# Kernel tuning notes

Measured on AMD Instinct MI355X. Metric: run time of the kernel, lower is better.

The kernel has to match this reference:

```python
import jax, jax.numpy as jnp
import numpy as np

KMAX = 16
NEG_INF = -1e9


def setup_inputs() -> dict:
    key = jax.random.key(0)
    ks = jax.random.split(key, 8)
    B, N, H = 65536, 512, 256
    L = KMAX + 1
    actions = jax.random.randint(ks[0], (B, L), 0, N + 1)  # values in [0, N], N == STOP
    rp = jax.random.uniform(ks[1], (B, 1), dtype=jnp.float32)
    s1 = 1.0 / np.sqrt(N + 3)
    s2 = 1.0 / np.sqrt(H)
    W1 = jax.random.normal(ks[2], (N + 3, H), dtype=jnp.float32) * s1
    b1 = jax.random.normal(ks[3], (H,), dtype=jnp.float32) * 0.01
    W2 = jax.random.normal(ks[4], (H, H), dtype=jnp.float32) * s2
    b2 = jax.random.normal(ks[5], (H,), dtype=jnp.float32) * 0.01
    Wh = jax.random.normal(ks[6], (H, N + 1), dtype=jnp.float32) * s2
    bh = jax.random.normal(ks[7], (N + 1,), dtype=jnp.float32) * 0.01
    return {"actions": actions, "rp": rp, "W1": W1, "b1": b1, "W2": W2, "b2": b2, "Wh": Wh, "bh": bh}


def reference(actions, rp, W1, b1, W2, b2, Wh, bh):
    B, L = actions.shape
    N = Wh.shape[1] - 1
    f32 = rp.dtype

    def step_fn(carry, a):
        sel_mask, k_sel, step, logpf = carry  # [B,N], [B,1], [B,1], [B]
        x = jnp.concatenate([sel_mask, k_sel, step, rp], axis=-1)  # [B, N+3]
        h = jax.nn.relu(x @ W1 + b1)
        h = jax.nn.relu(h @ W2 + b2)
        logits = h @ Wh + bh  # [B, N+1]
        k = k_sel[:, 0]
        full = (k >= KMAX).astype(f32)[:, None]
        mask_assets = (1.0 - sel_mask) * (1.0 - full)  # cannot re-add or exceed Kmax
        mask_stop = (k > 0).astype(f32)[:, None]       # cannot STOP on empty set
        mask = jnp.concatenate([mask_assets, mask_stop], axis=-1)
        logits = jnp.where(mask <= 0.0, NEG_INF, logits)
        logp = jax.nn.log_softmax(logits, axis=-1)
        alive = a >= 0
        a_safe = jnp.clip(a, 0, N)
        chosen = jnp.take_along_axis(logp, a_safe[:, None], axis=-1)[:, 0]
        logpf = logpf + jnp.where(alive, chosen, 0.0)
        stop = (a == N) & alive
        add = (alive & (~stop)).astype(f32)[:, None]
        # one_hot of N/-1 is all-zero, so only valid adds update sel_mask
        upd = jax.nn.one_hot(a_safe, N, dtype=f32) * add
        sel_mask = jnp.maximum(sel_mask, upd)
        k_sel = jnp.sum(sel_mask, axis=-1, keepdims=True)
        step = step + 1.0
        return (sel_mask, k_sel, step, logpf), None

    init = (jnp.zeros((B, N), f32), jnp.zeros((B, 1), f32), jnp.zeros((B, 1), f32), jnp.zeros((B,), f32))
    (_, _, _, logpf), _ = jax.lax.scan(step_fn, init, actions.T)  # scan over L steps
    return logpf
```

## Files before the change

kernel.cpp:

```cpp
#include <hip/hip_runtime.h>


#define NEG_INF (-1000000000.0f)
#define LOG2E 1.4426950408889634f
#define LN2   0.6931471805599453f

#define A_NEW  0x400

#define HST 1040
#define HKT 2080

typedef short bf16x8 __attribute__((ext_vector_type(8)));
typedef float f32x16 __attribute__((ext_vector_type(16)));

__device__ __forceinline__ unsigned short f2bf(float x){
  unsigned int u = __float_as_uint(x);
  u = (u + 0x7FFFu + ((u >> 16) & 1u)) >> 16;
  return (unsigned short)u;
}
__device__ __forceinline__ float bf2f(unsigned short h){
  return __uint_as_float(((unsigned int)h) << 16);
}
__device__ __forceinline__ unsigned int cvt_pk_bf16(float lo, float hi){
  unsigned int r;
  asm("v_cvt_pk_bf16_f32 %0, %1, %2" : "=v"(r) : "v"(lo), "v"(hi));
  return r;
}
__device__ __forceinline__ float4 ld4bf(const unsigned short* p){
  ushort4 u = *(const ushort4*)p;
  return make_float4(bf2f(u.x), bf2f(u.y), bf2f(u.z), bf2f(u.w));
}

__global__ void prep_kernel(const float* __restrict__ W2, const float* __restrict__ Wh,
                            unsigned short* __restrict__ w2f, unsigned short* __restrict__ whf,
                            float* __restrict__ whstop){
  int id = blockIdx.x * 256 + threadIdx.x;
  if (id < 8192){
    int lane = id & 63; int tile = id >> 6;
    int ntg = tile >> 4, kt = tile & 15;
    int col = ntg * 32 + (lane & 31);
    int k0  = kt * 16 + (lane >> 5) * 8;
    unsigned int u[4];
#pragma unroll
    for (int p = 0; p < 4; ++p){
      unsigned short lo = f2bf(W2[(k0 + 2*p    ) * 256 + col]);
      unsigned short hi = f2bf(W2[(k0 + 2*p + 1) * 256 + col]);
      u[p] = (unsigned int)lo | ((unsigned int)hi << 16);
    }
    *(uint4*)(w2f + (size_t)id * 8) = make_uint4(u[0], u[1], u[2], u[3]);
  } else if (id < 24576){
    int id2 = id - 8192;
    int lane = id2 & 63; int tile = id2 >> 6;
    int pt = tile >> 4, kt = tile & 15;
    int col = pt * 32 + (lane & 31);
    int k0  = kt * 16 + (lane >> 5) * 8;
    unsigned int u[4];
#pragma unroll
    for (int p = 0; p < 4; ++p){
      unsigned short lo = f2bf(Wh[(k0 + 2*p    ) * 513 + col] * LOG2E);
      unsigned short hi = f2bf(Wh[(k0 + 2*p + 1) * 513 + col] * LOG2E);
      u[p] = (unsigned int)lo | ((unsigned int)hi << 16);
    }
    *(uint4*)(whf + (size_t)id2 * 8) = make_uint4(u[0], u[1], u[2], u[3]);
  } else if (id < 24832){
    int k = id - 24576;
    whstop[k] = Wh[k * 513 + 512];
  }
}

__launch_bounds__(256, 4)
__global__ void gfn_kernel(const int* __restrict__ actions, const float* __restrict__ rp,
                           const float* __restrict__ W1, const float* __restrict__ b1,
                           const float* __restrict__ b2, const float* __restrict__ bh,
                           const unsigned short* __restrict__ w2f,
                           const unsigned short* __restrict__ whf,
                           const float* __restrict__ whstop,
                           float* __restrict__ out)
{
  __shared__ alignas(16) char h[32 * HST];
  __shared__ alignas(16) unsigned short c16[1024];
  __shared__ alignas(16) float bhl2[512];
  __shared__ alignas(16) float b2s[256];
  __shared__ alignas(16) unsigned short whst_h[256];
  __shared__ alignas(16) unsigned short amask[18][32];
  __shared__ alignas(16) float predsum[64];
  __shared__ alignas(16) float stopp[64];
  __shared__ alignas(16) unsigned short chosen16[64];

  const int tid  = threadIdx.x;
  const int wave = tid >> 6;
  const int lane = tid & 63;
  const int ln5  = lane & 31;
  const int lg2  = lane >> 5;
  const int base = blockIdx.x * 32;

  for (int i = tid; i < 1024; i += 256){
    int rrow = i >> 8, f = i & 255;
    float v = (rrow < 3) ? W1[(512 + rrow) * 256 + f] : b1[f];
    c16[i] = f2bf(v);
  }
  b2s[tid] = b2[tid];
  whst_h[tid] = f2bf(whstop[tid]);
  for (int i = tid; i < 512; i += 256){
    int pt = i >> 5, l2 = (i >> 4) & 1, r = i & 15;
    int col = pt * 32 + (r & 3) + 8 * (r >> 2) + 4 * l2;
    bhl2[i] = bh[col] * LOG2E;
  }
  const float stopbias = bh[512];
  if (tid < 64){ stopp[tid] = 0.f; predsum[tid] = 0.f; }
  int* acts = (int*)h;
  for (int i = tid; i < 544; i += 256) acts[i] = actions[base * 17 + i];
  float logpf = 0.f;
  uint4 selw_r = make_uint4(0u, 0u, 0u, 0u);
  __syncthreads();

  if (tid < 32){
    int s = tid, k = 0;
    for (int t = 0; t < 17; ++t){
      int a = acts[s * 17 + t];
      bool alive = (a >= 0);
      bool isnew = alive && (a < 512);
      if (isnew){
        for (int u = 0; u < t; ++u) if (acts[s * 17 + u] == a){ isnew = false; break; }
      }
      int av = alive ? a : 1023;
      amask[t][s] = (unsigned short)(av | (isnew ? A_NEW : 0) | (k << 11));
      if (isnew) ++k;
    }
    amask[17][s] = (unsigned short)(1023 | (k << 11));
  }
  unsigned int Spk[16];
#pragma unroll
  for (int j = 0; j < 16; ++j) Spk[j] = 0u;
  __syncthreads();

  const int aw_base = (lane >> 1) * HST + (lane & 1) * 8 + wave * 128;
  const int br_base = lg2 * HST;
  const int bw_base = wave * 8 * HST + lg2 * 8;
  const int cr_base = lg2 * HST + ln5 * 16;
  const int rpu = __builtin_amdgcn_readfirstlane(base + wave * 8);
  const unsigned lane8 = (unsigned)lane * 8u;
  const unsigned short* w2p0 = w2f + (unsigned)(wave * 2    ) * 8192u + lane8;
  const unsigned short* w2p1 = w2f + (unsigned)(wave * 2 + 1) * 8192u + lane8;

#pragma unroll 1
  for (int c = 0; c < 9; ++c){
    const int t = c * 2;

    {
      const float4 ck4 = ld4bf(&c16[lane * 4]);
      const float4 ct4 = ld4bf(&c16[256 + lane * 4]);
      const float4 cr4 = ld4bf(&c16[512 + lane * 4]);
      const float4 cb4 = ld4bf(&c16[768 + lane * 4]);
      float tf = (float)t;
      float c00 = cb4.x + tf * ct4.x, c01 = cb4.y + tf * ct4.y;
      float c02 = cb4.z + tf * ct4.z, c03 = cb4.w + tf * ct4.w;
#pragma unroll
      for (int s8 = 0; s8 < 8; ++s8){
        int s = wave * 8 + s8;
        float rv = rp[rpu + s8];
        int m0 = amask[t][s];
        int m1 = amask[t + 1][s];
        unsigned int pk0 = Spk[s8 * 2], pk1 = Spk[s8 * 2 + 1];
        float S0 = __uint_as_float(pk0 << 16);
        float S1 = __uint_as_float(pk0 & 0xFFFF0000u);
        float S2 = __uint_as_float(pk1 << 16);
        float S3 = __uint_as_float(pk1 & 0xFFFF0000u);
        float kf = (float)(m0 >> 11);
        float v0 = S0 + kf * ck4.x + rv * cr4.x + c00;
        float v1 = S1 + kf * ck4.y + rv * cr4.y + c01;
        float v2 = S2 + kf * ck4.z + rv * cr4.z + c02;
        float v3 = S3 + kf * ck4.w + rv * cr4.w + c03;
        *(uint2*)(h + aw_base + s8 * 16) =
            make_uint2(cvt_pk_bf16(fmaxf(v0,0.f), fmaxf(v1,0.f)),
                       cvt_pk_bf16(fmaxf(v2,0.f), fmaxf(v3,0.f)));
        float d0 = ct4.x, d1 = ct4.y, d2 = ct4.z, d3 = ct4.w;
        if (m0 & A_NEW){
          int a = m0 & 1023;
          float4 w = *(const float4*)(W1 + (size_t)a * 256 + lane * 4);
          S0 += w.x; S1 += w.y; S2 += w.z; S3 += w.w;
          d0 += w.x + ck4.x; d1 += w.y + ck4.y; d2 += w.z + ck4.z; d3 += w.w + ck4.w;
        }
        v0 += d0; v1 += d1; v2 += d2; v3 += d3;
        *(uint2*)(h + aw_base + 512 + s8 * 16) =
            make_uint2(cvt_pk_bf16(fmaxf(v0,0.f), fmaxf(v1,0.f)),
                       cvt_pk_bf16(fmaxf(v2,0.f), fmaxf(v3,0.f)));
        if (m1 & A_NEW){
          int a = m1 & 1023;
          float4 w = *(const float4*)(W1 + (size_t)a * 256 + lane * 4);
          S0 += w.x; S1 += w.y; S2 += w.z; S3 += w.w;
        }
        if ((m0 | m1) & A_NEW){
          Spk[s8 * 2]     = cvt_pk_bf16(S0, S1);
          Spk[s8 * 2 + 1] = cvt_pk_bf16(S2, S3);
        }
      }
    }
    __syncthreads();

#pragma unroll 1
    for (int q = 0; q < 2; ++q){
      const int rr = q * 32 + ln5;
      const int brq = br_base + rr * 16;
      f32x16 aB0, aB1;
#pragma unroll
      for (int i = 0; i < 16; ++i){ aB0[i] = 0.f; aB1[i] = 0.f; }
#pragma unroll 4
      for (int kt = 0; kt < 16; ++kt){
        bf16x8 sf = *(const bf16x8*)(h + brq + kt * HKT);
        bf16x8 w0 = *(const bf16x8*)(w2p0 + (unsigned)(kt * 512));
        bf16x8 w1 = *(const bf16x8*)(w2p1 + (unsigned)(kt * 512));
        aB0 = __builtin_amdgcn_mfma_f32_32x32x16_bf16(w0, sf, aB0, 0, 0, 0);
        aB1 = __builtin_amdgcn_mfma_f32_32x32x16_bf16(w1, sf, aB1, 0, 0, 0);
      }
      __syncthreads();
      const int bwq = bw_base + rr * 16;
      float sp = 0.f;
#pragma unroll
      for (int g = 0; g < 4; ++g){
        int f0 = wave * 64 + g * 8 + lg2 * 4;
        int f1 = f0 + 32;
        float4 bb0 = *(const float4*)&b2s[f0];
        float4 bb1 = *(const float4*)&b2s[f1];
        float4 ws0 = ld4bf(&whst_h[f0]);
        float4 ws1 = ld4bf(&whst_h[f1]);
        {
          float v0 = fmaxf(aB0[g*4+0] + bb0.x, 0.f), v1 = fmaxf(aB0[g*4+1] + bb0.y, 0.f);
          float v2 = fmaxf(aB0[g*4+2] + bb0.z, 0.f), v3 = fmaxf(aB0[g*4+3] + bb0.w, 0.f);
          sp += v0 * ws0.x + v1 * ws0.y + v2 * ws0.z + v3 * ws0.w;
          *(uint2*)(h + bwq + g * HST) = make_uint2(cvt_pk_bf16(v0, v1), cvt_pk_bf16(v2, v3));
        }
        {
          float v0 = fmaxf(aB1[g*4+0] + bb1.x, 0.f), v1 = fmaxf(aB1[g*4+1] + bb1.y, 0.f);
          float v2 = fmaxf(aB1[g*4+2] + bb1.z, 0.f), v3 = fmaxf(aB1[g*4+3] + bb1.w, 0.f);
          sp += v0 * ws1.x + v1 * ws1.y + v2 * ws1.z + v3 * ws1.w;
          *(uint2*)(h + bwq + (g + 4) * HST) = make_uint2(cvt_pk_bf16(v0, v1), cvt_pk_bf16(v2, v3));
        }
      }
      sp += __shfl_xor(sp, 32);
      if (lg2 == 0) atomicAdd(&stopp[rr], sp);
    }
    __syncthreads();

    {
      int mt  = amask[t][ln5];
      int mt1 = amask[t + 1][ln5];
      int av0 = mt & 1023, av1 = mt1 & 1023;
      int pa = (mt & A_NEW) ? av0 : -1;
      float sum0 = 0.f, sum1 = 0.f;
#pragma unroll 1
      for (int p = 0; p < 4; ++p){
        int pt = wave * 4 + p;
        const unsigned short* wp = whf + (unsigned)pt * 8192u + lane8;
        const float* bi = &bhl2[pt * 32 + lg2 * 16];
        float4 b0_ = *(const float4*)(bi);
        float4 b1_ = *(const float4*)(bi + 4);
        float4 b2_ = *(const float4*)(bi + 8);
        float4 b3_ = *(const float4*)(bi + 12);
        f32x16 a0, a1;
        a0[0]=b0_.x; a0[1]=b0_.y; a0[2]=b0_.z; a0[3]=b0_.w;
        a0[4]=b1_.x; a0[5]=b1_.y; a0[6]=b1_.z; a0[7]=b1_.w;
        a0[8]=b2_.x; a0[9]=b2_.y; a0[10]=b2_.z; a0[11]=b2_.w;
        a0[12]=b3_.x; a0[13]=b3_.y; a0[14]=b3_.z; a0[15]=b3_.w;
        a1 = a0;
#pragma unroll 4
        for (int kt = 0; kt < 16; ++kt){
          bf16x8 f0 = *(const bf16x8*)(h + cr_base + kt * HKT);
          bf16x8 f1 = *(const bf16x8*)(h + cr_base + 512 + kt * HKT);
          bf16x8 w = *(const bf16x8*)(wp + (unsigned)(kt * 512));
          a0 = __builtin_amdgcn_mfma_f32_32x32x16_bf16(w, f0, a0, 0, 0, 0);
          a1 = __builtin_amdgcn_mfma_f32_32x32x16_bf16(w, f1, a1, 0, 0, 0);
        }
        unsigned wlo = (p & 1) ? selw_r.y : selw_r.x;
        unsigned whi = (p & 1) ? selw_r.w : selw_r.z;
        unsigned word = (p & 2) ? whi : wlo;
        unsigned wsel = (word >> (lg2 * 16)) & 0xFFFFu;
        unsigned msk0 = (mt  & 0x8000) ? 0xFFFFu : wsel;
        unsigned msk1 = (mt1 & 0x8000) ? 0xFFFFu : wsel;
        if (pa >= 0 && (pa >> 5) == pt && (((pa >> 2) & 1) == lg2))
          msk1 |= 1u << ((pa & 3) | (((pa >> 3) & 3) << 2));
        int tr0 = (av0 < 512 && (av0 >> 5) == pt && (((av0 >> 2) & 1) == lg2))
                  ? ((av0 & 3) | (((av0 >> 3) & 3) << 2)) : -1;
        int tr1 = (av1 < 512 && (av1 >> 5) == pt && (((av1 >> 2) & 1) == lg2))
                  ? ((av1 & 3) | (((av1 >> 3) & 3) << 2)) : -1;
        float cv0 = 0.f, cv1 = 0.f;
#pragma unroll
        for (int r = 0; r < 16; ++r){
          float v0 = ((msk0 >> r) & 1u) ? NEG_INF : a0[r];
          float v1 = ((msk1 >> r) & 1u) ? NEG_INF : a1[r];
          sum0 += __builtin_amdgcn_exp2f(v0);
          sum1 += __builtin_amdgcn_exp2f(v1);
          if (r == tr0) cv0 = a0[r];
          if (r == tr1) cv1 = a1[r];
        }
        if (tr0 >= 0) chosen16[ln5]      = f2bf(cv0);
        if (tr1 >= 0) chosen16[32 + ln5] = f2bf(cv1);
      }
      sum0 += __shfl_xor(sum0, 32);
      sum1 += __shfl_xor(sum1, 32);
      if (lg2 == 0){
        atomicAdd(&predsum[ln5], sum0);
        atomicAdd(&predsum[32 + ln5], sum1);
      }
#pragma unroll
      for (int e = 0; e < 2; ++e){
        int m = e ? mt1 : mt;
        if ((m & A_NEW) && (((m & 1023) >> 7) == wave)){
          int av = m & 1023;
          int w2 = (av >> 5) & 3;
          unsigned bit = 1u << ((((av >> 2) & 1) << 4) | (av & 3) | (((av >> 3) & 3) << 2));
          if (w2 == 0) selw_r.x |= bit;
          else if (w2 == 1) selw_r.y |= bit;
          else if (w2 == 2) selw_r.z |= bit;
          else selw_r.w |= bit;
        }
      }
    }
    __syncthreads();

    if (tid < 32){
      int s = tid;
      int m0 = amask[t][s];
      int m1 = amask[t + 1][s];
      int av0 = m0 & 1023, av1 = m1 & 1023;
      int k0 = m0 >> 11, k1 = m1 >> 11;
      float stop0 = (k0 == 0) ? NEG_INF : stopp[s] + stopbias;
      float stop1 = (k1 == 0) ? NEG_INF : stopp[32 + s] + stopbias;
      {
        float tot = __expf(stop0) + predsum[s];
        float lse = __logf(tot);
        if (av0 != 1023){
          float ch;
          if (av0 == 512) ch = stop0;
          else {
            bool mskd = !(m0 & A_NEW) || (k0 >= 16);
            ch = mskd ? NEG_INF : bf2f(chosen16[s]) * LN2;
          }
          logpf += ch - lse;
        }
      }
      {
        float tot = __expf(stop1) + predsum[32 + s];
        float lse = __logf(tot);
        if (av1 != 1023){
          float ch;
          if (av1 == 512) ch = stop1;
          else {
            bool mskd = !(m1 & A_NEW) || (k1 >= 16);
            ch = mskd ? NEG_INF : bf2f(chosen16[32 + s]) * LN2;
          }
          logpf += ch - lse;
        }
      }
      stopp[s] = 0.f; stopp[32 + s] = 0.f;
      predsum[s] = 0.f; predsum[32 + s] = 0.f;
    }
    __syncthreads();
  }

  if (tid < 32) out[base + tid] = logpf;
}

extern "C" void kernel_launch(void* const* d_in, const int* in_sizes, int n_in,
                              void* d_out, int out_size, void* d_ws, size_t ws_size,
                              hipStream_t stream)
{
  const int*   actions = (const int*)d_in[0];
  const float* rp  = (const float*)d_in[1];
  const float* W1  = (const float*)d_in[2];
  const float* b1  = (const float*)d_in[3];
  const float* W2  = (const float*)d_in[4];
  const float* b2  = (const float*)d_in[5];
  const float* Wh  = (const float*)d_in[6];
  const float* bh  = (const float*)d_in[7];
  float* out = (float*)d_out;

  unsigned short* w2f = (unsigned short*)d_ws;
  unsigned short* whf = w2f + 65536;
  float* whstop = (float*)(whf + 131072);

  prep_kernel<<<97, 256, 0, stream>>>(W2, Wh, w2f, whf, whstop);
  gfn_kernel<<<2048, 256, 0, stream>>>(actions, rp, W1, b1, b2, bh, w2f, whf, whstop, out);
}
```

Measured before the change: 575.4 us.

## Defer per-step finalize into next chunk, pair head tiles, store head bias as bf16

Moves the per-sample log-softmax finalize out of its own barrier-separated phase and runs it inside the next chunk, after the layer-1 barrier. This removes one __syncthreads per chunk, and the last chunk is finalized after the loop. The head GEMM now handles two 32-column tiles per iteration, giving four independent MFMA accumulators that share each activation fragment load. The head bias is kept in LDS as bf16 to make room for the extra register pressure. The risks are more register use at 4 waves/SIMD occupancy and a small loss of bias precision.

```diff
diff --git a/kernel.cpp b/kernel.cpp
--- a/kernel.cpp
+++ b/kernel.cpp
@@ -79,7 +79,7 @@
 {
   __shared__ alignas(16) char h[32 * HST];
   __shared__ alignas(16) unsigned short c16[1024];
-  __shared__ alignas(16) float bhl2[512];
+  __shared__ alignas(16) unsigned short bhl216[512];
   __shared__ alignas(16) float b2s[256];
   __shared__ alignas(16) unsigned short whst_h[256];
   __shared__ alignas(16) unsigned short amask[18][32];
@@ -104,7 +104,7 @@
   for (int i = tid; i < 512; i += 256){
     int pt = i >> 5, l2 = (i >> 4) & 1, r = i & 15;
     int col = pt * 32 + (r & 3) + 8 * (r >> 2) + 4 * l2;
-    bhl2[i] = bh[col] * LOG2E;
+    bhl216[i] = f2bf(bh[col] * LOG2E);
   }
   const float stopbias = bh[512];
   if (tid < 64){ stopp[tid] = 0.f; predsum[tid] = 0.f; }
@@ -142,6 +142,44 @@
   const unsigned lane8 = (unsigned)lane * 8u;
   const unsigned short* w2p0 = w2f + (unsigned)(wave * 2    ) * 8192u + lane8;
   const unsigned short* w2p1 = w2f + (unsigned)(wave * 2 + 1) * 8192u + lane8;
+
+  auto finalize2 = [&](int tprev){
+    int s = tid;
+    int m0 = amask[tprev][s];
+    int m1 = amask[tprev + 1][s];
+    int av0 = m0 & 1023, av1 = m1 & 1023;
+    int k0 = m0 >> 11, k1 = m1 >> 11;
+    float stop0 = (k0 == 0) ? NEG_INF : stopp[s] + stopbias;
+    float stop1 = (k1 == 0) ? NEG_INF : stopp[32 + s] + stopbias;
+    {
+      float tot = __expf(stop0) + predsum[s];
+      float lse = __logf(tot);
+      if (av0 != 1023){
+        float ch;
+        if (av0 == 512) ch = stop0;
+        else {
+          bool mskd = !(m0 & A_NEW) || (k0 >= 16);
+          ch = mskd ? NEG_INF : bf2f(chosen16[s]) * LN2;
+        }
+        logpf += ch - lse;
+      }
+    }
+    {
+      float tot = __expf(stop1) + predsum[32 + s];
+      float lse = __logf(tot);
+      if (av1 != 1023){
+        float ch;
+        if (av1 == 512) ch = stop1;
+        else {
+          bool mskd = !(m1 & A_NEW) || (k1 >= 16);
+          ch = mskd ? NEG_INF : bf2f(chosen16[32 + s]) * LN2;
+        }
+        logpf += ch - lse;
+      }
+    }
+    stopp[s] = 0.f; stopp[32 + s] = 0.f;
+    predsum[s] = 0.f; predsum[32 + s] = 0.f;
+  };
 
 #pragma unroll 1
   for (int c = 0; c < 9; ++c){
@@ -198,6 +236,8 @@
     }
     __syncthreads();
 
+    if (c > 0 && tid < 32) finalize2(t - 2);
+
 #pragma unroll 1
     for (int q = 0; q < 2; ++q){
       const int rr = q * 32 + ln5;
@@ -249,52 +289,66 @@
       int pa = (mt & A_NEW) ? av0 : -1;
       float sum0 = 0.f, sum1 = 0.f;
 #pragma unroll 1
-      for (int p = 0; p < 4; ++p){
-        int pt = wave * 4 + p;
-        const unsigned short* wp = whf + (unsigned)pt * 8192u + lane8;
-        const float* bi = &bhl2[pt * 32 + lg2 * 16];
-        float4 b0_ = *(const float4*)(bi);
-        float4 b1_ = *(const float4*)(bi + 4);
-        float4 b2_ = *(const float4*)(bi + 8);
-        float4 b3_ = *(const float4*)(bi + 12);
-        f32x16 a0, a1;
-        a0[0]=b0_.x; a0[1]=b0_.y; a0[2]=b0_.z; a0[3]=b0_.w;
-        a0[4]=b1_.x; a0[5]=b1_.y; a0[6]=b1_.z; a0[7]=b1_.w;
-        a0[8]=b2_.x; a0[9]=b2_.y; a0[10]=b2_.z; a0[11]=b2_.w;
-        a0[12]=b3_.x; a0[13]=b3_.y; a0[14]=b3_.z; a0[15]=b3_.w;
-        a1 = a0;
+      for (int pp = 0; pp < 2; ++pp){
+        int pt0 = wave * 4 + pp * 2;
+        int pt1 = pt0 + 1;
+        const unsigned short* wp0 = whf + (unsigned)pt0 * 8192u + lane8;
+        const unsigned short* wp1 = wp0 + 8192u;
+        f32x16 a00, a01, a10, a11;
+        {
+          const unsigned short* bi0 = &bhl216[pt0 * 32 + lg2 * 16];
+          const unsigned short* bi1 = &bhl216[pt1 * 32 + lg2 * 16];
+#pragma unroll
+          for (int g = 0; g < 4; ++g){
+            float4 v0 = ld4bf(bi0 + g * 4);
+            float4 v1 = ld4bf(bi1 + g * 4);
+            a00[g*4+0]=v0.x; a00[g*4+1]=v0.y; a00[g*4+2]=v0.z; a00[g*4+3]=v0.w;
+            a10[g*4+0]=v1.x; a10[g*4+1]=v1.y; a10[g*4+2]=v1.z; a10[g*4+3]=v1.w;
+          }
+          a01 = a00; a11 = a10;
+        }
 #pragma unroll 4
         for (int kt = 0; kt < 16; ++kt){
           bf16x8 f0 = *(const bf16x8*)(h + cr_base + kt * HKT);
           bf16x8 f1 = *(const bf16x8*)(h + cr_base + 512 + kt * HKT);
-          bf16x8 w = *(const bf16x8*)(wp + (unsigned)(kt * 512));
-          a0 = __builtin_amdgcn_mfma_f32_32x32x16_bf16(w, f0, a0, 0, 0, 0);
-          a1 = __builtin_amdgcn_mfma_f32_32x32x16_bf16(w, f1, a1, 0, 0, 0);
-        }
-        unsigned wlo = (p & 1) ? selw_r.y : selw_r.x;
-        unsigned whi = (p & 1) ? selw_r.w : selw_r.z;
-        unsigned word = (p & 2) ? whi : wlo;
-        unsigned wsel = (word >> (lg2 * 16)) & 0xFFFFu;
-        unsigned msk0 = (mt  & 0x8000) ? 0xFFFFu : wsel;
-        unsigned msk1 = (mt1 & 0x8000) ? 0xFFFFu : wsel;
-        if (pa >= 0 && (pa >> 5) == pt && (((pa >> 2) & 1) == lg2))
-          msk1 |= 1u << ((pa & 3) | (((pa >> 3) & 3) << 2));
-        int tr0 = (av0 < 512 && (av0 >> 5) == pt && (((av0 >> 2) & 1) == lg2))
-                  ? ((av0 & 3) | (((av0 >> 3) & 3) << 2)) : -1;
-        int tr1 = (av1 < 512 && (av1 >> 5) == pt && (((av1 >> 2) & 1) == lg2))
-                  ? ((av1 & 3) | (((av1 >> 3) & 3) << 2)) : -1;
-        float cv0 = 0.f, cv1 = 0.f;
-#pragma unroll
-        for (int r = 0; r < 16; ++r){
-          float v0 = ((msk0 >> r) & 1u) ? NEG_INF : a0[r];
-          float v1 = ((msk1 >> r) & 1u) ? NEG_INF : a1[r];
-          sum0 += __builtin_amdgcn_exp2f(v0);
-          sum1 += __builtin_amdgcn_exp2f(v1);
-          if (r == tr0) cv0 = a0[r];
-          if (r == tr1) cv1 = a1[r];
-        }
-        if (tr0 >= 0) chosen16[ln5]      = f2bf(cv0);
-        if (tr1 >= 0) chosen16[32 + ln5] = f2bf(cv1);
+          bf16x8 w0 = *(const bf16x8*)(wp0 + (unsigned)(kt * 512));
+          bf16x8 w1 = *(const bf16x8*)(wp1 + (unsigned)(kt * 512));
+          a00 = __builtin_amdgcn_mfma_f32_32x32x16_bf16(w0, f0, a00, 0, 0, 0);
+          a01 = __builtin_amdgcn_mfma_f32_32x32x16_bf16(w0, f1, a01, 0, 0, 0);
+          a10 = __builtin_amdgcn_mfma_f32_32x32x16_bf16(w1, f0, a10, 0, 0, 0);
+          a11 = __builtin_amdgcn_mfma_f32_32x32x16_bf16(w1, f1, a11, 0, 0, 0);
+        }
+        unsigned word0 = pp ? selw_r.z : selw_r.x;
+        unsigned word1 = pp ? selw_r.w : selw_r.y;
+        unsigned wsel0 = (word0 >> (lg2 * 16)) & 0xFFFFu;
+        unsigned wsel1 = (word1 >> (lg2 * 16)) & 0xFFFFu;
+#pragma unroll
+        for (int e = 0; e < 2; ++e){
+          int pt = e ? pt1 : pt0;
+          unsigned wsel = e ? wsel1 : wsel0;
+          unsigned msk0 = (mt  & 0x8000) ? 0xFFFFu : wsel;
+          unsigned msk1 = (mt1 & 0x8000) ? 0xFFFFu : wsel;
+          if (pa >= 0 && (pa >> 5) == pt && (((pa >> 2) & 1) == lg2))
+            msk1 |= 1u << ((pa & 3) | (((pa >> 3) & 3) << 2));
+          int tr0 = (av0 < 512 && (av0 >> 5) == pt && (((av0 >> 2) & 1) == lg2))
+                    ? ((av0 & 3) | (((av0 >> 3) & 3) << 2)) : -1;
+          int tr1 = (av1 < 512 && (av1 >> 5) == pt && (((av1 >> 2) & 1) == lg2))
+                    ? ((av1 & 3) | (((av1 >> 3) & 3) << 2)) : -1;
+          const f32x16& x0 = e ? a10 : a00;
+          const f32x16& x1 = e ? a11 : a01;
+          float cv0 = 0.f, cv1 = 0.f;
+#pragma unroll
+          for (int r = 0; r < 16; ++r){
+            float v0 = ((msk0 >> r) & 1u) ? NEG_INF : x0[r];
+            float v1 = ((msk1 >> r) & 1u) ? NEG_INF : x1[r];
+            sum0 += __builtin_amdgcn_exp2f(v0);
+            sum1 += __builtin_amdgcn_exp2f(v1);
+            if (r == tr0) cv0 = x0[r];
+            if (r == tr1) cv1 = x1[r];
+          }
+          if (tr0 >= 0) chosen16[ln5]      = f2bf(cv0);
+          if (tr1 >= 0) chosen16[32 + ln5] = f2bf(cv1);
+        }
       }
       sum0 += __shfl_xor(sum0, 32);
       sum1 += __shfl_xor(sum1, 32);
@@ -317,48 +371,12 @@
       }
     }
     __syncthreads();
-
-    if (tid < 32){
-      int s = tid;
-      int m0 = amask[t][s];
-      int m1 = amask[t + 1][s];
-      int av0 = m0 & 1023, av1 = m1 & 1023;
-      int k0 = m0 >> 11, k1 = m1 >> 11;
-      float stop0 = (k0 == 0) ? NEG_INF : stopp[s] + stopbias;
-      float stop1 = (k1 == 0) ? NEG_INF : stopp[32 + s] + stopbias;
-      {
-        float tot = __expf(stop0) + predsum[s];
-        float lse = __logf(tot);
-        if (av0 != 1023){
-          float ch;
-          if (av0 == 512) ch = stop0;
-          else {
-            bool mskd = !(m0 & A_NEW) || (k0 >= 16);
-            ch = mskd ? NEG_INF : bf2f(chosen16[s]) * LN2;
-          }
-          logpf += ch - lse;
-        }
-      }
-      {
-        float tot = __expf(stop1) + predsum[32 + s];
-        float lse = __logf(tot);
-        if (av1 != 1023){
-          float ch;
-          if (av1 == 512) ch = stop1;
-          else {
-            bool mskd = !(m1 & A_NEW) || (k1 >= 16);
-            ch = mskd ? NEG_INF : bf2f(chosen16[32 + s]) * LN2;
-          }
-          logpf += ch - lse;
-        }
-      }
-      stopp[s] = 0.f; stopp[32 + s] = 0.f;
-      predsum[s] = 0.f; predsum[32 + s] = 0.f;
-    }
-    __syncthreads();
-  }
-
-  if (tid < 32) out[base + tid] = logpf;
+  }
+
+  if (tid < 32){
+    finalize2(16);
+    out[base + tid] = logpf;
+  }
 }
 
 extern "C" void kernel_launch(void* const* d_in, const int* in_sizes, int n_in,
```

Result: slower. 1.254 ms (+117.9%).

## Process one timestep per iteration to halve LDS and raise occupancy

Applied to the files above, without the earlier changes.

The old kernel handled two timesteps per outer iteration, holding activations for 64 rows (two steps × 32 samples) in shared memory. The new one does a single step per iteration, which halves the activation buffer stride and all the per-step scratch arrays. It also folds the per-step log-softmax finalize into the start of the next iteration, which removes one block barrier per step, and raises launch bounds to 5 blocks per CU. The trade-off is twice as many outer iterations and barriers, and each iteration's MFMA batches only half as many rows, so every weight-tile load is reused across fewer rows.

```diff
diff --git a/kernel.cpp b/kernel.cpp
--- a/kernel.cpp
+++ b/kernel.cpp
@@ -7,8 +7,8 @@
 
 #define A_NEW  0x400
 
-#define HST 1040
-#define HKT 2080
+#define HST 528
+#define HKT 1056
 
 typedef short bf16x8 __attribute__((ext_vector_type(8)));
 typedef float f32x16 __attribute__((ext_vector_type(16)));
@@ -68,7 +68,7 @@
   }
 }
 
-__launch_bounds__(256, 4)
+__launch_bounds__(256, 5)
 __global__ void gfn_kernel(const int* __restrict__ actions, const float* __restrict__ rp,
                            const float* __restrict__ W1, const float* __restrict__ b1,
                            const float* __restrict__ b2, const float* __restrict__ bh,
@@ -82,10 +82,10 @@
   __shared__ alignas(16) float bhl2[512];
   __shared__ alignas(16) float b2s[256];
   __shared__ alignas(16) unsigned short whst_h[256];
-  __shared__ alignas(16) unsigned short amask[18][32];
-  __shared__ alignas(16) float predsum[64];
-  __shared__ alignas(16) float stopp[64];
-  __shared__ alignas(16) unsigned short chosen16[64];
+  __shared__ alignas(16) unsigned short amask[17][32];
+  __shared__ alignas(16) float predsum[32];
+  __shared__ alignas(16) float stopp[32];
+  __shared__ alignas(16) unsigned short chosen16[32];
 
   const int tid  = threadIdx.x;
   const int wave = tid >> 6;
@@ -107,7 +107,7 @@
     bhl2[i] = bh[col] * LOG2E;
   }
   const float stopbias = bh[512];
-  if (tid < 64){ stopp[tid] = 0.f; predsum[tid] = 0.f; }
+  if (tid < 32){ stopp[tid] = 0.f; predsum[tid] = 0.f; }
   int* acts = (int*)h;
   for (int i = tid; i < 544; i += 256) acts[i] = actions[base * 17 + i];
   float logpf = 0.f;
@@ -127,7 +127,6 @@
       amask[t][s] = (unsigned short)(av | (isnew ? A_NEW : 0) | (k << 11));
       if (isnew) ++k;
     }
-    amask[17][s] = (unsigned short)(1023 | (k << 11));
   }
   unsigned int Spk[16];
 #pragma unroll
@@ -135,8 +134,8 @@
   __syncthreads();
 
   const int aw_base = (lane >> 1) * HST + (lane & 1) * 8 + wave * 128;
-  const int br_base = lg2 * HST;
-  const int bw_base = wave * 8 * HST + lg2 * 8;
+  const int br_base = lg2 * HST + ln5 * 16;
+  const int bw_base = wave * 8 * HST + lg2 * 8 + ln5 * 16;
   const int cr_base = lg2 * HST + ln5 * 16;
   const int rpu = __builtin_amdgcn_readfirstlane(base + wave * 8);
   const unsigned lane8 = (unsigned)lane * 8u;
@@ -144,8 +143,27 @@
   const unsigned short* w2p1 = w2f + (unsigned)(wave * 2 + 1) * 8192u + lane8;
 
 #pragma unroll 1
-  for (int c = 0; c < 9; ++c){
-    const int t = c * 2;
+  for (int t = 0; t < 17; ++t){
+
+    if (t > 0 && tid < 32){
+      int s = tid;
+      int m = amask[t - 1][s];
+      int av = m & 1023;
+      int k = m >> 11;
+      float stop = (k == 0) ? NEG_INF : stopp[s] + stopbias;
+      float tot = __expf(stop) + predsum[s];
+      float lse = __logf(tot);
+      if (av != 1023){
+        float ch;
+        if (av == 512) ch = stop;
+        else {
+          bool mskd = !(m & A_NEW) || (k >= 16);
+          ch = mskd ? NEG_INF : bf2f(chosen16[s]) * LN2;
+        }
+        logpf += ch - lse;
+      }
+      stopp[s] = 0.f; predsum[s] = 0.f;
+    }
 
     {
       const float4 ck4 = ld4bf(&c16[lane * 4]);
@@ -160,7 +178,6 @@
         int s = wave * 8 + s8;
         float rv = rp[rpu + s8];
         int m0 = amask[t][s];
-        int m1 = amask[t + 1][s];
         unsigned int pk0 = Spk[s8 * 2], pk1 = Spk[s8 * 2 + 1];
         float S0 = __uint_as_float(pk0 << 16);
         float S1 = __uint_as_float(pk0 & 0xFFFF0000u);
@@ -174,23 +191,10 @@
         *(uint2*)(h + aw_base + s8 * 16) =
             make_uint2(cvt_pk_bf16(fmaxf(v0,0.f), fmaxf(v1,0.f)),
                        cvt_pk_bf16(fmaxf(v2,0.f), fmaxf(v3,0.f)));
-        float d0 = ct4.x, d1 = ct4.y, d2 = ct4.z, d3 = ct4.w;
         if (m0 & A_NEW){
           int a = m0 & 1023;
           float4 w = *(const float4*)(W1 + (size_t)a * 256 + lane * 4);
           S0 += w.x; S1 += w.y; S2 += w.z; S3 += w.w;
-          d0 += w.x + ck4.x; d1 += w.y + ck4.y; d2 += w.z + ck4.z; d3 += w.w + ck4.w;
-        }
-        v0 += d0; v1 += d1; v2 += d2; v3 += d3;
-        *(uint2*)(h + aw_base + 512 + s8 * 16) =
-            make_uint2(cvt_pk_bf16(fmaxf(v0,0.f), fmaxf(v1,0.f)),
-                       cvt_pk_bf16(fmaxf(v2,0.f), fmaxf(v3,0.f)));
-        if (m1 & A_NEW){
-          int a = m1 & 1023;
-          float4 w = *(const float4*)(W1 + (size_t)a * 256 + lane * 4);
-          S0 += w.x; S1 += w.y; S2 += w.z; S3 += w.w;
-        }
-        if ((m0 | m1) & A_NEW){
           Spk[s8 * 2]     = cvt_pk_bf16(S0, S1);
           Spk[s8 * 2 + 1] = cvt_pk_bf16(S2, S3);
         }
@@ -198,23 +202,19 @@
     }
     __syncthreads();
 
-#pragma unroll 1
-    for (int q = 0; q < 2; ++q){
-      const int rr = q * 32 + ln5;
-      const int brq = br_base + rr * 16;
+    {
       f32x16 aB0, aB1;
 #pragma unroll
       for (int i = 0; i < 16; ++i){ aB0[i] = 0.f; aB1[i] = 0.f; }
 #pragma unroll 4
       for (int kt = 0; kt < 16; ++kt){
-        bf16x8 sf = *(const bf16x8*)(h + brq + kt * HKT);
+        bf16x8 sf = *(const bf16x8*)(h + br_base + kt * HKT);
         bf16x8 w0 = *(const bf16x8*)(w2p0 + (unsigned)(kt * 512));
         bf16x8 w1 = *(const bf16x8*)(w2p1 + (unsigned)(kt * 512));
         aB0 = __builtin_amdgcn_mfma_f32_32x32x16_bf16(w0, sf, aB0, 0, 0, 0);
         aB1 = __builtin_amdgcn_mfma_f32_32x32x16_bf16(w1, sf, aB1, 0, 0, 0);
       }
       __syncthreads();
-      const int bwq = bw_base + rr * 16;
       float sp = 0.f;
 #pragma unroll
       for (int g = 0; g < 4; ++g){
@@ -228,137 +228,105 @@
           float v0 = fmaxf(aB0[g*4+0] + bb0.x, 0.f), v1 = fmaxf(aB0[g*4+1] + bb0.y, 0.f);
           float v2 = fmaxf(aB0[g*4+2] + bb0.z, 0.f), v3 = fmaxf(aB0[g*4+3] + bb0.w, 0.f);
           sp += v0 * ws0.x + v1 * ws0.y + v2 * ws0.z + v3 * ws0.w;
-          *(uint2*)(h + bwq + g * HST) = make_uint2(cvt_pk_bf16(v0, v1), cvt_pk_bf16(v2, v3));
+          *(uint2*)(h + bw_base + g * HST) = make_uint2(cvt_pk_bf16(v0, v1), cvt_pk_bf16(v2, v3));
         }
         {
           float v0 = fmaxf(aB1[g*4+0] + bb1.x, 0.f), v1 = fmaxf(aB1[g*4+1] + bb1.y, 0.f);
           float v2 = fmaxf(aB1[g*4+2] + bb1.z, 0.f), v3 = fmaxf(aB1[g*4+3] + bb1.w, 0.f);
           sp += v0 * ws1.x + v1 * ws1.y + v2 * ws1.z + v3 * ws1.w;
-          *(uint2*)(h + bwq + (g + 4) * HST) = make_uint2(cvt_pk_bf16(v0, v1), cvt_pk_bf16(v2, v3));
+          *(uint2*)(h + bw_base + (g + 4) * HST) = make_uint2(cvt_pk_bf16(v0, v1), cvt_pk_bf16(v2, v3));
         }
       }
       sp += __shfl_xor(sp, 32);
-      if (lg2 == 0) atomicAdd(&stopp[rr], sp);
+      if (lg2 == 0) atomicAdd(&stopp[ln5], sp);
     }
     __syncthreads();
 
     {
-      int mt  = amask[t][ln5];
-      int mt1 = amask[t + 1][ln5];
-      int av0 = mt & 1023, av1 = mt1 & 1023;
-      int pa = (mt & A_NEW) ? av0 : -1;
-      float sum0 = 0.f, sum1 = 0.f;
+      int mt = amask[t][ln5];
+      int av = mt & 1023;
+      float sum = 0.f;
 #pragma unroll 1
-      for (int p = 0; p < 4; ++p){
-        int pt = wave * 4 + p;
-        const unsigned short* wp = whf + (unsigned)pt * 8192u + lane8;
-        const float* bi = &bhl2[pt * 32 + lg2 * 16];
-        float4 b0_ = *(const float4*)(bi);
-        float4 b1_ = *(const float4*)(bi + 4);
-        float4 b2_ = *(const float4*)(bi + 8);
-        float4 b3_ = *(const float4*)(bi + 12);
+      for (int pp = 0; pp < 2; ++pp){
+        int pt0 = wave * 4 + pp * 2;
+        int pt1 = pt0 + 1;
+        const unsigned short* wp0 = whf + (unsigned)pt0 * 8192u + lane8;
+        const unsigned short* wp1 = wp0 + 8192u;
         f32x16 a0, a1;
-        a0[0]=b0_.x; a0[1]=b0_.y; a0[2]=b0_.z; a0[3]=b0_.w;
-        a0[4]=b1_.x; a0[5]=b1_.y; a0[6]=b1_.z; a0[7]=b1_.w;
-        a0[8]=b2_.x; a0[9]=b2_.y; a0[10]=b2_.z; a0[11]=b2_.w;
-        a0[12]=b3_.x; a0[13]=b3_.y; a0[14]=b3_.z; a0[15]=b3_.w;
-        a1 = a0;
+        {
+          const float* bi0 = &bhl2[pt0 * 32 + lg2 * 16];
+          const float* bi1 = &bhl2[pt1 * 32 + lg2 * 16];
+#pragma unroll
+          for (int g = 0; g < 4; ++g){
+            float4 u0 = *(const float4*)(bi0 + g * 4);
+            float4 u1 = *(const float4*)(bi1 + g * 4);
+            a0[g*4+0]=u0.x; a0[g*4+1]=u0.y; a0[g*4+2]=u0.z; a0[g*4+3]=u0.w;
+            a1[g*4+0]=u1.x; a1[g*4+1]=u1.y; a1[g*4+2]=u1.z; a1[g*4+3]=u1.w;
+          }
+        }
 #pragma unroll 4
         for (int kt = 0; kt < 16; ++kt){
           bf16x8 f0 = *(const bf16x8*)(h + cr_base + kt * HKT);
-          bf16x8 f1 = *(const bf16x8*)(h + cr_base + 512 + kt * HKT);
-          bf16x8 w = *(const bf16x8*)(wp + (unsigned)(kt * 512));
-          a0 = __builtin_amdgcn_mfma_f32_32x32x16_bf16(w, f0, a0, 0, 0, 0);
-          a1 = __builtin_amdgcn_mfma_f32_32x32x16_bf16(w, f1, a1, 0, 0, 0);
-        }
-        unsigned wlo = (p & 1) ? selw_r.y : selw_r.x;
-        unsigned whi = (p & 1) ? selw_r.w : selw_r.z;
-        unsigned word = (p & 2) ? whi : wlo;
-        unsigned wsel = (word >> (lg2 * 16)) & 0xFFFFu;
-        unsigned msk0 = (mt  & 0x8000) ? 0xFFFFu : wsel;
-        unsigned msk1 = (mt1 & 0x8000) ? 0xFFFFu : wsel;
-        if (pa >= 0 && (pa >> 5) == pt && (((pa >> 2) & 1) == lg2))
-          msk1 |= 1u << ((pa & 3) | (((pa >> 3) & 3) << 2));
-        int tr0 = (av0 < 512 && (av0 >> 5) == pt && (((av0 >> 2) & 1) == lg2))
-                  ? ((av0 & 3) | (((av0 >> 3) & 3) << 2)) : -1;
-        int tr1 = (av1 < 512 && (av1 >> 5) == pt && (((av1 >> 2) & 1) == lg2))
-                  ? ((av1 & 3) | (((av1 >> 3) & 3) << 2)) : -1;
+          bf16x8 w0 = *(const bf16x8*)(wp0 + (unsigned)(kt * 512));
+          bf16x8 w1 = *(const bf16x8*)(wp1 + (unsigned)(kt * 512));
+          a0 = __builtin_amdgcn_mfma_f32_32x32x16_bf16(w0, f0, a0, 0, 0, 0);
+          a1 = __builtin_amdgcn_mfma_f32_32x32x16_bf16(w1, f0, a1, 0, 0, 0);
+        }
+        unsigned word0 = pp ? selw_r.z : selw_r.x;
+        unsigned word1 = pp ? selw_r.w : selw_r.y;
+        unsigned wsel0 = (word0 >> (lg2 * 16)) & 0xFFFFu;
+        unsigned wsel1 = (word1 >> (lg2 * 16)) & 0xFFFFu;
+        unsigned msk0 = (mt & 0x8000) ? 0xFFFFu : wsel0;
+        unsigned msk1 = (mt & 0x8000) ? 0xFFFFu : wsel1;
+        bool gl = (av < 512) && (((av >> 2) & 1) == lg2);
+        int tr0 = (gl && (av >> 5) == pt0) ? ((av & 3) | (((av >> 3) & 3) << 2)) : -1;
+        int tr1 = (gl && (av >> 5) == pt1) ? ((av & 3) | (((av >> 3) & 3) << 2)) : -1;
         float cv0 = 0.f, cv1 = 0.f;
 #pragma unroll
         for (int r = 0; r < 16; ++r){
           float v0 = ((msk0 >> r) & 1u) ? NEG_INF : a0[r];
           float v1 = ((msk1 >> r) & 1u) ? NEG_INF : a1[r];
-          sum0 += __builtin_amdgcn_exp2f(v0);
-          sum1 += __builtin_amdgcn_exp2f(v1);
+          sum += __builtin_amdgcn_exp2f(v0);
+          sum += __builtin_amdgcn_exp2f(v1);
           if (r == tr0) cv0 = a0[r];
           if (r == tr1) cv1 = a1[r];
         }
-        if (tr0 >= 0) chosen16[ln5]      = f2bf(cv0);
-        if (tr1 >= 0) chosen16[32 + ln5] = f2bf(cv1);
-      }
-      sum0 += __shfl_xor(sum0, 32);
-      sum1 += __shfl_xor(sum1, 32);
-      if (lg2 == 0){
-        atomicAdd(&predsum[ln5], sum0);
-        atomicAdd(&predsum[32 + ln5], sum1);
-      }
-#pragma unroll
-      for (int e = 0; e < 2; ++e){
-        int m = e ? mt1 : mt;
-        if ((m & A_NEW) && (((m & 1023) >> 7) == wave)){
-          int av = m & 1023;
-          int w2 = (av >> 5) & 3;
-          unsigned bit = 1u << ((((av >> 2) & 1) << 4) | (av & 3) | (((av >> 3) & 3) << 2));
-          if (w2 == 0) selw_r.x |= bit;
-          else if (w2 == 1) selw_r.y |= bit;
-          else if (w2 == 2) selw_r.z |= bit;
-          else selw_r.w |= bit;
-        }
+        if (tr0 >= 0) chosen16[ln5] = f2bf(cv0);
+        if (tr1 >= 0) chosen16[ln5] = f2bf(cv1);
+      }
+      sum += __shfl_xor(sum, 32);
+      if (lg2 == 0) atomicAdd(&predsum[ln5], sum);
+      if ((mt & A_NEW) && ((av >> 7) == wave)){
+        int w2 = (av >> 5) & 3;
+        unsigned bit = 1u << ((((av >> 2) & 1) << 4) | (av & 3) | (((av >> 3) & 3) << 2));
+        if (w2 == 0) selw_r.x |= bit;
+        else if (w2 == 1) selw_r.y |= bit;
+        else if (w2 == 2) selw_r.z |= bit;
+        else selw_r.w |= bit;
       }
     }
     __syncthreads();
-
-    if (tid < 32){
-      int s = tid;
-      int m0 = amask[t][s];
-      int m1 = amask[t + 1][s];
-      int av0 = m0 & 1023, av1 = m1 & 1023;
-      int k0 = m0 >> 11, k1 = m1 >> 11;
-      float stop0 = (k0 == 0) ? NEG_INF : stopp[s] + stopbias;
-      float stop1 = (k1 == 0) ? NEG_INF : stopp[32 + s] + stopbias;
-      {
-        float tot = __expf(stop0) + predsum[s];
-        float lse = __logf(tot);
-        if (av0 != 1023){
-          float ch;
-          if (av0 == 512) ch = stop0;
-          else {
-            bool mskd = !(m0 & A_NEW) || (k0 >= 16);
-            ch = mskd ? NEG_INF : bf2f(chosen16[s]) * LN2;
-          }
-          logpf += ch - lse;
-        }
-      }
-      {
-        float tot = __expf(stop1) + predsum[32 + s];
-        float lse = __logf(tot);
-        if (av1 != 1023){
-          float ch;
-          if (av1 == 512) ch = stop1;
-          else {
-            bool mskd = !(m1 & A_NEW) || (k1 >= 16);
-            ch = mskd ? NEG_INF : bf2f(chosen16[32 + s]) * LN2;
-          }
-          logpf += ch - lse;
-        }
-      }
-      stopp[s] = 0.f; stopp[32 + s] = 0.f;
-      predsum[s] = 0.f; predsum[32 + s] = 0.f;
-    }
-    __syncthreads();
-  }
-
-  if (tid < 32) out[base + tid] = logpf;
+  }
+
+  if (tid < 32){
+    int s = tid;
+    int m = amask[16][s];
+    int av = m & 1023;
+    int k = m >> 11;
+    float stop = (k == 0) ? NEG_INF : stopp[s] + stopbias;
+    float tot = __expf(stop) + predsum[s];
+    float lse = __logf(tot);
+    if (av != 1023){
+      float ch;
+      if (av == 512) ch = stop;
+      else {
+        bool mskd = !(m & A_NEW) || (k >= 16);
+        ch = mskd ? NEG_INF : bf2f(chosen16[s]) * LN2;
+      }
+      logpf += ch - lse;
+    }
+    out[base + tid] = logpf;
+  }
 }
 
 extern "C" void kernel_launch(void* const* d_in, const int* in_sizes, int n_in,
```

New measurement: 624.5 us. 8.5% more time.
